# Kernel tuning notes

Hardware: AMD Instinct MI355X
Metric: run time of the kernel (lower is better)

Reference implementation:

```python
import jax, jax.numpy as jnp
import numpy as np

N = 80000
E = 1280000
C_IN, HID, C_OUT = 3, 64, 1
DEPTH = 3
KS = [40000, 20000, 10000]  # ceil(0.5 * n) per pooling level
EPS = 1e-5


def gcn_conv(x, W, src, dst, ew, n, fill=2.0):
    # PyG GCNConv with add_self_loops=True; improved => self-loop weight fill=2.0
    h = x @ W                                           # [n, F]
    deg = jax.ops.segment_sum(ew, dst, num_segments=n) + fill
    dinv = jax.lax.rsqrt(deg)
    norm = dinv[src] * ew * dinv[dst]                   # [E]
    agg = jax.ops.segment_sum(norm[:, None] * h[src], dst, num_segments=n)
    return agg + (fill * dinv * dinv)[:, None] * h      # self-loop term


def batchnorm(x, gamma, beta):
    # BatchNorm1d in training mode: biased batch stats over the node dim
    mu = jnp.mean(x, axis=0)
    var = jnp.var(x, axis=0)
    return gamma * (x - mu) * jax.lax.rsqrt(var + EPS) + beta


def gcn_block(x, src, dst, ew, n, W, gamma, beta, fill=2.0):
    return jax.nn.relu(batchnorm(gcn_conv(x, W, src, dst, ew, n, fill), gamma, beta))


def topk_pool(x, src, dst, ew, w, k):
    # TopKPooling with ReLU nonlinearity: score = relu(x.w / ||w||)
    n = x.shape[0]
    score = jax.nn.relu(x @ w / jnp.linalg.norm(w))
    sc, perm = jax.lax.top_k(score, k)
    xk = x[perm] * sc[:, None]
    # filter_adj with fixed edge count: invalid edges get weight 0 (no-op in GCN)
    mapping = jnp.full((n,), -1, dtype=src.dtype).at[perm].set(
        jnp.arange(k, dtype=src.dtype))
    ns, nd = mapping[src], mapping[dst]
    valid = (ns >= 0) & (nd >= 0)
    ns = jnp.where(valid, ns, 0)
    nd = jnp.where(valid, nd, 0)
    new_ew = jnp.where(valid, ew, jnp.zeros((), ew.dtype))
    return xk, ns, nd, new_ew, perm


def _forward(x, edge_index, Wd, gd, bd, pw, Wu, gu, bu, W_out):
    src, dst = edge_index[0], edge_index[1]
    ew = jnp.ones(src.shape, x.dtype)
    n = x.shape[0]
    x = gcn_block(x, src, dst, ew, n, Wd[0], gd[0], bd[0])
    xs, sds, ews, perms = [x], [(src, dst)], [ew], []
    for i in range(DEPTH):
        x, src, dst, ew, perm = topk_pool(x, src, dst, ew, pw[i], KS[i])
        x = gcn_block(x, src, dst, ew, KS[i], Wd[i + 1], gd[i + 1], bd[i + 1])
        if i < DEPTH - 1:
            xs.append(x); sds.append((src, dst)); ews.append(ew)
        perms.append(perm)
    for i in range(DEPTH):
        j = DEPTH - 1 - i
        res = xs[j]; src, dst = sds[j]; ew = ews[j]; perm = perms[j]
        up = jnp.zeros_like(res).at[perm].set(x)
        x = res + up
        if i < DEPTH - 1:
            x = gcn_block(x, src, dst, ew, res.shape[0], Wu[i], gu[i], bu[i])
        else:
            x = jax.nn.sigmoid(
                gcn_conv(x, W_out, src, dst, ew, res.shape[0], fill=1.0))
    return x


def setup_inputs() -> dict:
    key = jax.random.key(0)
    ks = jax.random.split(key, 16)
    nrm = lambda k, shape: jax.random.normal(k, shape, jnp.float32) * 0.1
    inp = {
        "x": jax.random.normal(ks[0], (N, C_IN), jnp.float32),
        "edge_index": jax.random.randint(ks[1], (2, E), 0, N, jnp.int32),
    }
    dims = [(C_IN, HID)] + [(HID, HID)] * DEPTH
    ki = 2
    for l, (a, b) in enumerate(dims):
        inp[f"W_d{l}"] = nrm(ks[ki], (a, b)); ki += 1
        inp[f"g_d{l}"] = jnp.ones((b,), jnp.float32)
        inp[f"b_d{l}"] = jnp.zeros((b,), jnp.float32)
    for l in range(DEPTH):
        inp[f"pw{l}"] = nrm(ks[ki], (HID,)); ki += 1
    for l in range(DEPTH - 1):
        inp[f"W_u{l}"] = nrm(ks[ki], (HID, HID)); ki += 1
        inp[f"g_u{l}"] = jnp.ones((HID,), jnp.float32)
        inp[f"b_u{l}"] = jnp.zeros((HID,), jnp.float32)
    inp["W_out"] = nrm(ks[ki], (HID, C_OUT))
    return inp


def reference(x, edge_index, W_d0, g_d0, b_d0, W_d1, g_d1, b_d1, W_d2, g_d2,
              b_d2, W_d3, g_d3, b_d3, pw0, pw1, pw2, W_u0, g_u0, b_u0,
              W_u1, g_u1, b_u1, W_out):
    Wd = [W_d0, W_d1, W_d2, W_d3]
    gd = [g_d0, g_d1, g_d2, g_d3]
    bd = [b_d0, b_d1, b_d2, b_d3]
    pw = [pw0, pw1, pw2]
    Wu = [W_u0, W_u1]
    gu = [g_u0, g_u1]
    bu = [b_u0, b_u1]
    return _forward(x, edge_index, Wd, gd, bd, pw, Wu, gu, bu, W_out)
```

## Files before the change

kernel.cpp:

```cpp
#include <hip/hip_runtime.h>
#include <cstdint>
#include <utility>

#define NN0 80000
#define NE 1280000
#define MMB_GRID 2048
#define EB 2048
#define ENB 625

static inline int cdiv(int a, int b){ return (a+b-1)/b; }

__global__ void k_conv64(const int* __restrict__ rp, const int* __restrict__ col,
                         const float* __restrict__ dinv, const float* __restrict__ x,
                         const float* __restrict__ W, float* __restrict__ out,
                         float* __restrict__ part, int n){
  __shared__ float yl[4][64];
  __shared__ float ls[64], lq[64];
  int lane = threadIdx.x & 63, w = threadIdx.x >> 6;
  if (threadIdx.x < 64){ ls[threadIdx.x] = 0.f; lq[threadIdx.x] = 0.f; }
  __syncthreads();
  float sa = 0.f, sq = 0.f;
  int wid = blockIdx.x*4 + w, nw = gridDim.x*4;
  for (int i = wid; i < n; i += nw){
    int beg = rp[i], end = rp[i+1];
    float di = dinv[i];
    float y = 0.f;
    int j = beg;
    for (; j + 4 <= end; j += 4){
      int s0 = col[j], s1 = col[j+1], s2 = col[j+2], s3 = col[j+3];
      float y0 = dinv[s0]*x[s0*64+lane];
      float y1 = dinv[s1]*x[s1*64+lane];
      float y2 = dinv[s2]*x[s2*64+lane];
      float y3 = dinv[s3]*x[s3*64+lane];
      y += (y0+y1) + (y2+y3);
    }
    for (; j < end; j++){ int s = col[j]; y += dinv[s]*x[s*64+lane]; }
    y = di*y + 2.f*di*di*x[i*64+lane];
    yl[w][lane] = y;
    float acc = 0.f;
    #pragma unroll
    for (int k2 = 0; k2 < 64; k2++)
      acc += yl[w][k2]*W[k2*64+lane];
    out[i*64+lane] = acc;
    sa += acc; sq += acc*acc;
  }
  atomicAdd(&ls[lane], sa); atomicAdd(&lq[lane], sq);
  __syncthreads();
  if (threadIdx.x < 128)
    part[blockIdx.x*128 + threadIdx.x] =
      (threadIdx.x < 64) ? ls[threadIdx.x] : lq[threadIdx.x-64];
}

__global__ void k_conv3(const int* __restrict__ rp, const int* __restrict__ col,
                        const float* __restrict__ dinv, const float* __restrict__ x,
                        const float* __restrict__ W, float* __restrict__ out,
                        float* __restrict__ part, int n){
  __shared__ float ls[64], lq[64];
  int lane = threadIdx.x & 63, w = threadIdx.x >> 6;
  if (threadIdx.x < 64){ ls[threadIdx.x] = 0.f; lq[threadIdx.x] = 0.f; }
  __syncthreads();
  float wf0 = W[lane], wf1 = W[64+lane], wf2 = W[128+lane];
  float sa = 0.f, sq = 0.f;
  int wid = blockIdx.x*4 + w, nw = gridDim.x*4;
  for (int i = wid; i < n; i += nw){
    int beg = rp[i], end = rp[i+1];
    float a0 = 0.f, a1 = 0.f, a2 = 0.f;
    for (int j = beg + lane; j < end; j += 64){
      int s2 = col[j];
      float ds = dinv[s2];
      a0 += ds*x[s2*3+0]; a1 += ds*x[s2*3+1]; a2 += ds*x[s2*3+2];
    }
    for (int o = 32; o > 0; o >>= 1){
      a0 += __shfl_xor(a0, o); a1 += __shfl_xor(a1, o); a2 += __shfl_xor(a2, o);
    }
    float di = dinv[i];
    float sl = 2.f*di*di;
    a0 = di*a0 + sl*x[i*3+0];
    a1 = di*a1 + sl*x[i*3+1];
    a2 = di*a2 + sl*x[i*3+2];
    float s = a0*wf0 + a1*wf1 + a2*wf2;
    out[i*64+lane] = s; sa += s; sq += s*s;
  }
  atomicAdd(&ls[lane], sa); atomicAdd(&lq[lane], sq);
  __syncthreads();
  if (threadIdx.x < 128)
    part[blockIdx.x*128 + threadIdx.x] =
      (threadIdx.x < 64) ? ls[threadIdx.x] : lq[threadIdx.x-64];
}

__global__ void k_stats_reduce(const float* __restrict__ part, float* __restrict__ stats){
  int c = blockIdx.x, lane = threadIdx.x;
  float s = 0.f;
  for (int b = lane; b < MMB_GRID; b += 64) s += part[b*128 + c];
  for (int o = 32; o > 0; o >>= 1) s += __shfl_xor(s, o);
  if (lane == 0) stats[c] = s;
}

__global__ void k_matvec(const float* __restrict__ x, const float* __restrict__ W,
                         float* __restrict__ h1, int n){
  int lane = threadIdx.x & 63, w = threadIdx.x >> 6;
  int wid = blockIdx.x*4 + w, nw = gridDim.x*4;
  float wv = W[lane];
  for (int i = wid; i < n; i += nw){
    float v = x[i*64+lane]*wv;
    for (int o = 32; o > 0; o >>= 1) v += __shfl_xor(v, o);
    if (lane == 0) h1[i] = v;
  }
}

__global__ void k_ehist6(const int* __restrict__ key, int* __restrict__ hist, int shift){
  __shared__ int lh[64];
  if (threadIdx.x < 64) lh[threadIdx.x] = 0;
  __syncthreads();
  int base = blockIdx.x*EB + threadIdx.x;
  #pragma unroll
  for (int u = 0; u < 8; u++)
    atomicAdd(&lh[(key[base + u*256] >> shift) & 63], 1);
  __syncthreads();
  if (threadIdx.x < 64) hist[threadIdx.x*ENB + blockIdx.x] = lh[threadIdx.x];
}

__global__ void k_escatter6(const int* __restrict__ keyin, const int* __restrict__ valin,
                            int* __restrict__ keyout, int* __restrict__ valout,
                            const int* __restrict__ hist, int shift){
  __shared__ int dbase[64], run[64], wcnt[4][64];
  int t = threadIdx.x, lane = t & 63, w = t >> 6;
  if (t < 64){ dbase[t] = hist[t*ENB + blockIdx.x]; run[t] = 0; }
  __syncthreads();
  for (int u = 0; u < 8; u++){
    if (t < 64){ wcnt[0][t]=0; wcnt[1][t]=0; wcnt[2][t]=0; wcnt[3][t]=0; }
    __syncthreads();
    int g = blockIdx.x*EB + u*256 + t;
    int kk = keyin[g], vv = valin[g];
    int d = (kk >> shift) & 63;
    unsigned long long m = ~0ull;
    #pragma unroll
    for (int b = 0; b < 6; b++){
      unsigned long long bal = __ballot((d >> b) & 1);
      m &= ((d >> b) & 1) ? bal : ~bal;
    }
    int rnk = __popcll(m & ((1ull << lane) - 1ull));
    if (rnk == 0) wcnt[w][d] = __popcll(m);
    __syncthreads();
    int off2 = run[d] + rnk;
    for (int w2 = 0; w2 < w; w2++) off2 += wcnt[w2][d];
    int pos = dbase[d] + off2;
    keyout[pos] = kk; valout[pos] = vv;
    __syncthreads();
    if (t < 64) run[t] += wcnt[0][t] + wcnt[1][t] + wcnt[2][t] + wcnt[3][t];
    __syncthreads();
  }
}

__global__ void k_rp_search(const int* __restrict__ skey, int* __restrict__ rp,
                            float* __restrict__ dinvA, float* __restrict__ dinvB, int n){
  int i = blockIdx.x*blockDim.x + threadIdx.x;
  if (i >= n) return;
  int lo = 0, hi = NE;
  while (lo < hi){ int mid = (lo+hi)>>1; if (skey[mid] < i) lo = mid+1; else hi = mid; }
  int a = lo;
  lo = a; hi = NE;
  while (lo < hi){ int mid = (lo+hi)>>1; if (skey[mid] < i+1) lo = mid+1; else hi = mid; }
  int b2 = lo;
  rp[i] = a;
  if (i == n-1) rp[n] = NE;
  float deg = (float)(b2 - a);
  dinvA[i] = 1.0f/sqrtf(deg + 2.f);
  dinvB[i] = 1.0f/sqrtf(deg + 1.f);
}

__global__ void k_scan_part(const int* __restrict__ in, int* __restrict__ bsum, int n){
  __shared__ int ws[256];
  int base = blockIdx.x*2048 + threadIdx.x*8;
  int s = 0;
  #pragma unroll
  for (int u = 0; u < 8; u++){ int i = base+u; if (i < n) s += in[i]; }
  ws[threadIdx.x] = s; __syncthreads();
  for (int st = 128; st > 0; st >>= 1){
    if (threadIdx.x < st) ws[threadIdx.x] += ws[threadIdx.x+st];
    __syncthreads();
  }
  if (threadIdx.x == 0) bsum[blockIdx.x] = ws[0];
}

__global__ void k_scan_fin_rp(const int* __restrict__ in, const int* __restrict__ bsum, int nb,
                              int* __restrict__ rp, float* __restrict__ dinvA, int n){
  __shared__ int bws[256]; __shared__ int ws[256];
  int t = threadIdx.x;
  bws[t] = (t < nb) ? bsum[t] : 0; __syncthreads();
  for (int st = 1; st < 256; st <<= 1){
    int a = (t >= st) ? bws[t-st] : 0; __syncthreads();
    bws[t] += a; __syncthreads();
  }
  int blockoff = (blockIdx.x == 0) ? 0 : bws[blockIdx.x-1];
  int base = blockIdx.x*2048 + t*8;
  int v[8]; int s = 0;
  #pragma unroll
  for (int u = 0; u < 8; u++){ int i = base+u; v[u] = (i < n) ? in[i] : 0; s += v[u]; }
  ws[t] = s; __syncthreads();
  for (int st = 1; st < 256; st <<= 1){
    int a = (t >= st) ? ws[t-st] : 0; __syncthreads();
    ws[t] += a; __syncthreads();
  }
  int off = blockoff + ws[t] - s;
  #pragma unroll
  for (int u = 0; u < 8; u++){
    int i = base+u;
    if (i < n){
      rp[i] = off; off += v[u];
      dinvA[i] = 1.0f/sqrtf((float)v[u] + 2.f);
      if (i == n-1) rp[n] = off;
    }
  }
}

__global__ void k_scan_fin_flat(int* __restrict__ data, const int* __restrict__ bsum, int nb, int n){
  __shared__ int bws[256]; __shared__ int ws[256];
  int t = threadIdx.x;
  bws[t] = (t < nb) ? bsum[t] : 0; __syncthreads();
  for (int st = 1; st < 256; st <<= 1){
    int a = (t >= st) ? bws[t-st] : 0; __syncthreads();
    bws[t] += a; __syncthreads();
  }
  int blockoff = (blockIdx.x == 0) ? 0 : bws[blockIdx.x-1];
  int base = blockIdx.x*2048 + t*8;
  int v[8]; int s = 0;
  #pragma unroll
  for (int u = 0; u < 8; u++){ int i = base+u; v[u] = (i < n) ? data[i] : 0; s += v[u]; }
  ws[t] = s; __syncthreads();
  for (int st = 1; st < 256; st <<= 1){
    int a = (t >= st) ? ws[t-st] : 0; __syncthreads();
    ws[t] += a; __syncthreads();
  }
  int off = blockoff + ws[t] - s;
  #pragma unroll
  for (int u = 0; u < 8; u++){
    int i = base+u;
    if (i < n){ data[i] = off; off += v[u]; }
  }
}

__global__ void k_hist_mapped(const int* __restrict__ rp_p, const int* __restrict__ col_p,
                              const int* __restrict__ mapv, int* __restrict__ indeg, int np){
  int d = blockIdx.x*blockDim.x + threadIdx.x;
  if (d >= np) return;
  int md = mapv[d];
  if (md < 0) return;
  int c = 0, e = rp_p[d+1];
  int j = rp_p[d];
  for (; j + 4 <= e; j += 4){
    int c0 = (mapv[col_p[j]]   >= 0);
    int c1 = (mapv[col_p[j+1]] >= 0);
    int c2 = (mapv[col_p[j+2]] >= 0);
    int c3 = (mapv[col_p[j+3]] >= 0);
    c += (c0+c1) + (c2+c3);
  }
  for (; j < e; j++) if (mapv[col_p[j]] >= 0) c++;
  indeg[md] = c;
}
__global__ void k_scatter_mapped(const int* __restrict__ rp_p, const int* __restrict__ col_p,
                                 const int* __restrict__ mapv, const int* __restrict__ rp_c,
                                 int* __restrict__ col_c, int np){
  int d = blockIdx.x*blockDim.x + threadIdx.x;
  if (d >= np) return;
  int md = mapv[d];
  if (md < 0) return;
  int pos = rp_c[md], e = rp_p[d+1];
  int j = rp_p[d];
  for (; j + 4 <= e; j += 4){
    int m0 = mapv[col_p[j]], m1 = mapv[col_p[j+1]];
    int m2 = mapv[col_p[j+2]], m3 = mapv[col_p[j+3]];
    if (m0 >= 0) col_c[pos++] = m0;
    if (m1 >= 0) col_c[pos++] = m1;
    if (m2 >= 0) col_c[pos++] = m2;
    if (m3 >= 0) col_c[pos++] = m3;
  }
  for (; j < e; j++){
    int ms = mapv[col_p[j]];
    if (ms >= 0) col_c[pos++] = ms;
  }
}

__global__ void k_gather_sig(const int* __restrict__ rp, const int* __restrict__ col,
                             const float* __restrict__ dinv, const float* __restrict__ h1,
                             float* __restrict__ out, int n){
  int i = blockIdx.x*blockDim.x + threadIdx.x;
  if (i >= n) return;
  int beg = rp[i], end = rp[i+1];
  float di = dinv[i];
  float acc = 0.f;
  int j = beg;
  for (; j + 4 <= end; j += 4){
    int s0 = col[j], s1 = col[j+1], s2 = col[j+2], s3 = col[j+3];
    float v0 = dinv[s0]*h1[s0];
    float v1 = dinv[s1]*h1[s1];
    float v2 = dinv[s2]*h1[s2];
    float v3 = dinv[s3]*h1[s3];
    acc += (v0+v1) + (v2+v3);
  }
  for (; j < end; j++) acc += dinv[col[j]]*h1[col[j]];
  float v = di*acc + di*di*h1[i];
  out[i] = 1.f/(1.f+expf(-v));
}

__global__ void k_bnrelu_scatter(const float* __restrict__ x, const float* __restrict__ stats,
                                 const float* __restrict__ gamma, const float* __restrict__ beta,
                                 const int* __restrict__ perm, float* __restrict__ res, int n){
  int t = blockIdx.x*blockDim.x + threadIdx.x;
  if (t >= n*64) return;
  int r = t >> 6, f = t & 63;
  float inv_n = 1.0f/(float)n;
  float mu = stats[f]*inv_n;
  float var = stats[64+f]*inv_n - mu*mu;
  float v = gamma[f]*(x[t]-mu)*(1.0f/sqrtf(var+1e-5f)) + beta[f];
  res[perm[r]*64+f] += fmaxf(v, 0.f);
}

__global__ void k_bnrelu_score(float* __restrict__ x, const float* __restrict__ stats,
                               const float* __restrict__ gamma, const float* __restrict__ beta,
                               const float* __restrict__ pw,
                               float* __restrict__ score, unsigned* __restrict__ key,
                               int* __restrict__ idx, int n, int P){
  int lane = threadIdx.x & 63, w = threadIdx.x >> 6;
  int wid = blockIdx.x*4 + w, nw = gridDim.x*4;
  float inv_n = 1.f/(float)n;
  float mu = stats[lane]*inv_n;
  float var = stats[64+lane]*inv_n - mu*mu;
  float gs = gamma[lane]*(1.f/sqrtf(var+1e-5f));
  float bt = beta[lane];
  float pv = pw[lane];
  float q = pv*pv;
  for (int o = 32; o > 0; o >>= 1) q += __shfl_xor(q, o);
  float qn = 1.f/sqrtf(q);
  for (int i = wid; i < n; i += nw){
    float v = fmaxf(gs*(x[i*64+lane]-mu)+bt, 0.f);
    x[i*64+lane] = v;
    float s = v*pv;
    for (int o = 32; o > 0; o >>= 1) s += __shfl_xor(s, o);
    if (lane == 0){
      float sc = fmaxf(s*qn, 0.f);
      score[i] = sc; key[i] = ~__float_as_uint(sc); idx[i] = i;
    }
  }
  for (int g = n + wid; g < P; g += nw)
    if (lane == 0){ key[g] = 0xFFFFFFFFu; idx[g] = 0; }
}

__global__ void k_radix_hist(const unsigned* __restrict__ key, int* __restrict__ hist,
                             int shift, int nblk){
  __shared__ int lh[256];
  lh[threadIdx.x] = 0; __syncthreads();
  int base = blockIdx.x*1024 + threadIdx.x;
  #pragma unroll
  for (int u = 0; u < 4; u++){
    unsigned d = (key[base + u*256] >> shift) & 255u;
    atomicAdd(&lh[d], 1);
  }
  __syncthreads();
  hist[threadIdx.x*nblk + blockIdx.x] = lh[threadIdx.x];
}

__global__ void k_radix_scatter(const unsigned* __restrict__ keyin, const int* __restrict__ idxin,
                                unsigned* __restrict__ keyout, int* __restrict__ idxout,
                                const int* __restrict__ hist, int shift, int nblk){
  __shared__ int dbase[256], run[256], sc[256];
  __shared__ int wcnt[4][256];
  int t = threadIdx.x, lane = t & 63, w = t >> 6;
  int pre = 0, tot = 0;
  for (int b = 0; b < nblk; b++){
    int v = hist[t*nblk + b];
    if (b < blockIdx.x) pre += v;
    tot += v;
  }
  sc[t] = tot; __syncthreads();
  for (int st = 1; st < 256; st <<= 1){
    int a = (t >= st) ? sc[t-st] : 0; __syncthreads();
    sc[t] += a; __syncthreads();
  }
  dbase[t] = sc[t] - tot + pre;
  run[t] = 0;
  for (int u = 0; u < 4; u++){
    wcnt[0][t] = 0; wcnt[1][t] = 0; wcnt[2][t] = 0; wcnt[3][t] = 0;
    __syncthreads();
    int g = blockIdx.x*1024 + u*256 + t;
    unsigned kk = keyin[g]; int id = idxin[g];
    unsigned d = (kk >> shift) & 255u;
    unsigned long long m = ~0ull;
    #pragma unroll
    for (int b = 0; b < 8; b++){
      unsigned long long bal = __ballot((d >> b) & 1u);
      m &= ((d >> b) & 1u) ? bal : ~bal;
    }
    int rnk = __popcll(m & ((1ull << lane) - 1ull));
    if (rnk == 0) wcnt[w][d] = __popcll(m);
    __syncthreads();
    int off2 = run[d] + rnk;
    for (int w2 = 0; w2 < w; w2++) off2 += wcnt[w2][d];
    int pos = dbase[d] + off2;
    keyout[pos] = kk; idxout[pos] = id;
    __syncthreads();
    run[t] += wcnt[0][t] + wcnt[1][t] + wcnt[2][t] + wcnt[3][t];
    __syncthreads();
  }
}

__global__ void k_select_gather(const int* __restrict__ idxs, const float* __restrict__ x,
                                const float* __restrict__ score, int* __restrict__ perm,
                                int* __restrict__ mapv, float* __restrict__ xk, int n, int k){
  int t = blockIdx.x*blockDim.x + threadIdx.x;
  if (t < n){
    int i = idxs[t];
    mapv[i] = (t < k) ? t : -1;
    if (t < k) perm[t] = i;
  }
  if (t < k*64){
    int r = t >> 6, f = t & 63;
    int i = idxs[r];
    xk[t] = x[i*64+f]*score[i];
  }
}

extern "C" void kernel_launch(void* const* d_in, const int* in_sizes, int n_in,
                              void* d_out, int out_size, void* d_ws, size_t ws_size,
                              hipStream_t stream) {
  const float* x_in = (const float*)d_in[0];
  const int* ei = (const int*)d_in[1];
  const int* src0 = ei;
  const int* dst0 = ei + NE;
  const float* W_d[4] = {(const float*)d_in[2],(const float*)d_in[5],(const float*)d_in[8],(const float*)d_in[11]};
  const float* g_d[4] = {(const float*)d_in[3],(const float*)d_in[6],(const float*)d_in[9],(const float*)d_in[12]};
  const float* b_d[4] = {(const float*)d_in[4],(const float*)d_in[7],(const float*)d_in[10],(const float*)d_in[13]};
  const float* pw[3]  = {(const float*)d_in[14],(const float*)d_in[15],(const float*)d_in[16]};
  const float* W_u[2] = {(const float*)d_in[17],(const float*)d_in[20]};
  const float* g_u[2] = {(const float*)d_in[18],(const float*)d_in[21]};
  const float* b_u[2] = {(const float*)d_in[19],(const float*)d_in[22]};
  const float* W_out  = (const float*)d_in[23];
  float* out = (float*)d_out;

  float* base = (float*)d_ws;
  size_t off = 0;
  auto alloc = [&](size_t nf){ float* p = base + off; off += nf; return p; };
  float* x0 = alloc(5120000);
  float* x1 = alloc(2560000);
  float* x2 = alloc(1280000);
  float* x3 = alloc(640000);
  float* A  = alloc(2560000);
  int* col0 = (int*)alloc(NE);
  int* col1 = (int*)alloc(NE);
  int* col2 = (int*)alloc(NE);
  int* col3 = (int*)alloc(NE);
  int* ek1 = (int*)alloc(NE);
  int* ev1 = (int*)alloc(NE);
  int* ek2 = (int*)alloc(NE);
  int* ev2 = (int*)alloc(NE);
  int* rp0 = (int*)alloc(80001);
  int* rp1 = (int*)alloc(40001);
  int* rp2 = (int*)alloc(20001);
  int* rp3 = (int*)alloc(10001);
  int* indeg  = (int*)alloc(NN0);
  float* dinv0  = alloc(NN0);
  float* dinv0f = alloc(NN0);
  float* dinv1  = alloc(40000);
  float* dinv2  = alloc(20000);
  float* dinv3  = alloc(10000);
  float* score = alloc(NN0);
  int* mapv = (int*)alloc(NN0);
  int* p0 = (int*)alloc(40000);
  int* p1 = (int*)alloc(20000);
  int* p2 = (int*)alloc(10000);
  float* stats = alloc(128);
  float* part  = alloc(MMB_GRID*128);
  unsigned* keyA = (unsigned*)alloc(81920);
  unsigned* keyB = (unsigned*)alloc(81920);
  int* idxA = (int*)alloc(81920);
  int* idxB = (int*)alloc(81920);
  int* hist = (int*)alloc(81920);
  int* ehist = (int*)alloc(64*ENB);
  int* bsum = (int*)alloc(256);
  (void)ws_size; (void)in_sizes; (void)n_in; (void)out_size;

  const int B = 256;

  auto scan_flat = [&](int* data, int n2){
    int nb = cdiv(n2, 2048);
    k_scan_part    <<<nb, 256, 0, stream>>>(data, bsum, n2);
    k_scan_fin_flat<<<nb, 256, 0, stream>>>(data, bsum, nb, n2);
  };
  auto scan_csr = [&](const int* indeg_, int* rp, float* dv, int n2){
    int nb = cdiv(n2, 2048);
    k_scan_part  <<<nb, 256, 0, stream>>>(indeg_, bsum, n2);
    k_scan_fin_rp<<<nb, 256, 0, stream>>>(indeg_, bsum, nb, rp, dv, n2);
  };

  auto conv = [&](const float* xin, const float* W, int n,
                  const int* rp, const int* col, const float* dv, float* dstb){
    k_conv64<<<MMB_GRID, B, 0, stream>>>(rp, col, dv, xin, W, dstb, part, n);
    k_stats_reduce<<<128, 64, 0, stream>>>(part, stats);
  };

  auto pool = [&](float* xb, const float* g, const float* bt, const float* w,
                  int n, int k, int* pm, float* xk){
    int nblk = cdiv(n, 1024), P = nblk*1024;
    k_bnrelu_score<<<1024, B, 0, stream>>>(xb, stats, g, bt, w, score, keyA, idxA, n, P);
    unsigned* ka = keyA; int* ia = idxA; unsigned* kb = keyB; int* ib = idxB;
    for (int pass = 0; pass < 4; pass++){
      k_radix_hist   <<<nblk, 256, 0, stream>>>(ka, hist, pass*8, nblk);
      k_radix_scatter<<<nblk, 256, 0, stream>>>(ka, ia, kb, ib, hist, pass*8, nblk);
      std::swap(ka, kb); std::swap(ia, ib);
    }
    k_select_gather<<<cdiv(k*64,B), B, 0, stream>>>(ia, xb, score, pm, mapv, xk, n, k);
  };

  auto csr_mapped = [&](const int* rp_p, const int* col_p, int np, int nc,
                        int* rp_c, int* col_c, float* dv){
    k_hist_mapped<<<cdiv(np,B), B, 0, stream>>>(rp_p, col_p, mapv, indeg, np);
    scan_csr(indeg, rp_c, dv, nc);
    k_scatter_mapped<<<cdiv(np,B), B, 0, stream>>>(rp_p, col_p, mapv, rp_c, col_c, np);
  };

  k_ehist6   <<<ENB, B, 0, stream>>>(dst0, ehist, 0);
  scan_flat(ehist, 64*ENB);
  k_escatter6<<<ENB, B, 0, stream>>>(dst0, src0, ek1, ev1, ehist, 0);
  k_ehist6   <<<ENB, B, 0, stream>>>(ek1, ehist, 6);
  scan_flat(ehist, 64*ENB);
  k_escatter6<<<ENB, B, 0, stream>>>(ek1, ev1, ek2, ev2, ehist, 6);
  k_ehist6   <<<ENB, B, 0, stream>>>(ek2, ehist, 12);
  scan_flat(ehist, 64*ENB);
  k_escatter6<<<ENB, B, 0, stream>>>(ek2, ev2, ek1, col0, ehist, 12);
  k_rp_search<<<cdiv(NN0,B), B, 0, stream>>>(ek1, rp0, dinv0, dinv0f, NN0);

  k_conv3<<<MMB_GRID, B, 0, stream>>>(rp0, col0, dinv0, x_in, W_d[0], x0, part, NN0);
  k_stats_reduce<<<128, 64, 0, stream>>>(part, stats);
  pool(x0, g_d[0], b_d[0], pw[0], NN0, 40000, p0, A);
  csr_mapped(rp0, col0, NN0, 40000, rp1, col1, dinv1);

  conv(A, W_d[1], 40000, rp1, col1, dinv1, x1);
  pool(x1, g_d[1], b_d[1], pw[1], 40000, 20000, p1, A);
  csr_mapped(rp1, col1, 40000, 20000, rp2, col2, dinv2);

  conv(A, W_d[2], 20000, rp2, col2, dinv2, x2);
  pool(x2, g_d[2], b_d[2], pw[2], 20000, 10000, p2, A);
  csr_mapped(rp2, col2, 20000, 10000, rp3, col3, dinv3);

  conv(A, W_d[3], 10000, rp3, col3, dinv3, x3);

  k_bnrelu_scatter<<<cdiv(10000*64,B), B, 0, stream>>>(x3, stats, g_d[3], b_d[3], p2, x2, 10000);
  conv(x2, W_u[0], 20000, rp2, col2, dinv2, A);
  k_bnrelu_scatter<<<cdiv(20000*64,B), B, 0, stream>>>(A, stats, g_u[0], b_u[0], p1, x1, 20000);
  conv(x1, W_u[1], 40000, rp1, col1, dinv1, A);
  k_bnrelu_scatter<<<cdiv(40000*64,B), B, 0, stream>>>(A, stats, g_u[1], b_u[1], p0, x0, 40000);

  float* h1 = score;
  k_matvec<<<512, B, 0, stream>>>(x0, W_out, h1, NN0);
  k_gather_sig<<<cdiv(NN0,B), B, 0, stream>>>(rp0, col0, dinv0f, h1, out, NN0);
}
```

Before: 740.8 us.

## Build CSR via atomic counting, fuse radix histograms and BN stats reductions

The 3-pass 6-bit radix sort that built the initial CSR is replaced by an atomic degree count, a scan and an atomic-cursor scatter. BatchNorm statistics now go straight into per-layer global slots through atomics, which removes the separate stats-reduce kernels. Radix-sort histograms for top-k are built inside the score kernel and the previous scatter pass, so the standalone histogram kernels are gone. Together these cut kernel launches and extra passes over memory. In exchange, the neighbour order within each CSR row becomes nondeterministic, so float summation order varies between runs, and global atomic contention goes up.

```diff
diff --git a/kernel.cpp b/kernel.cpp
--- a/kernel.cpp
+++ b/kernel.cpp
@@ -1,19 +1,89 @@
 #include <hip/hip_runtime.h>
 #include <cstdint>
-#include <utility>
 
 #define NN0 80000
 #define NE 1280000
 #define MMB_GRID 2048
-#define EB 2048
-#define ENB 625
+#define HPSTRIDE 20480
 
 static inline int cdiv(int a, int b){ return (a+b-1)/b; }
+
+__global__ void k_init(float* stats6, int* indeg){
+  int t = blockIdx.x*blockDim.x + threadIdx.x;
+  if (t < 768) stats6[t] = 0.f;
+  for (int i = t; i < NN0; i += gridDim.x*blockDim.x) indeg[i] = 0;
+}
+
+__global__ void k_deg0(const int* __restrict__ dst, int* __restrict__ indeg){
+  for (int e = blockIdx.x*blockDim.x + threadIdx.x; e < NE; e += gridDim.x*blockDim.x)
+    atomicAdd(&indeg[dst[e]], 1);
+}
+
+__global__ void k_escat0(const int* __restrict__ dst, const int* __restrict__ srcv,
+                         int* __restrict__ cur, int* __restrict__ col){
+  for (int e = blockIdx.x*blockDim.x + threadIdx.x; e < NE; e += gridDim.x*blockDim.x){
+    int d = dst[e];
+    int pos = atomicAdd(&cur[d], 1);
+    col[pos] = srcv[e];
+  }
+}
+
+__global__ void k_scan_part(const int* __restrict__ in, int* __restrict__ bsum, int n){
+  __shared__ int ws[256];
+  int base = blockIdx.x*2048 + threadIdx.x*8;
+  int s = 0;
+  #pragma unroll
+  for (int u = 0; u < 8; u++){ int i = base+u; if (i < n) s += in[i]; }
+  ws[threadIdx.x] = s; __syncthreads();
+  for (int st = 128; st > 0; st >>= 1){
+    if (threadIdx.x < st) ws[threadIdx.x] += ws[threadIdx.x+st];
+    __syncthreads();
+  }
+  if (threadIdx.x == 0) bsum[blockIdx.x] = ws[0];
+}
+
+__global__ void k_scan_fin_rp(const int* __restrict__ in, const int* __restrict__ bsum, int nb,
+                              int* __restrict__ rp, int* __restrict__ cur,
+                              float* __restrict__ dinvA, float* __restrict__ dinvB, int n){
+  __shared__ int bws[256]; __shared__ int ws[256];
+  int t = threadIdx.x;
+  bws[t] = (t < nb) ? bsum[t] : 0; __syncthreads();
+  for (int st = 1; st < 256; st <<= 1){
+    int a = (t >= st) ? bws[t-st] : 0; __syncthreads();
+    bws[t] += a; __syncthreads();
+  }
+  int blockoff = (blockIdx.x == 0) ? 0 : bws[blockIdx.x-1];
+  int base = blockIdx.x*2048 + t*8;
+  int v[8]; int s = 0;
+  #pragma unroll
+  for (int u = 0; u < 8; u++){ int i = base+u; v[u] = (i < n) ? in[i] : 0; s += v[u]; }
+  ws[t] = s; __syncthreads();
+  for (int st = 1; st < 256; st <<= 1){
+    int a = (t >= st) ? ws[t-st] : 0; __syncthreads();
+    ws[t] += a; __syncthreads();
+  }
+  int off = blockoff + ws[t] - s;
+  #pragma unroll
+  for (int u = 0; u < 8; u++){
+    int i = base+u;
+    if (i < n){
+      rp[i] = off;
+      if (cur) cur[i] = off;
+      off += v[u];
+      dinvA[i] = 1.0f/sqrtf((float)v[u] + 2.f);
+      if (dinvB) dinvB[i] = 1.0f/sqrtf((float)v[u] + 1.f);
+      if (i == n-1) rp[n] = off;
+    }
+  }
+}
+
 
 __global__ void k_conv64(const int* __restrict__ rp, const int* __restrict__ col,
                          const float* __restrict__ dinv, const float* __restrict__ x,
                          const float* __restrict__ W, float* __restrict__ out,
-                         float* __restrict__ part, int n){
+                         float* __restrict__ statsS, int* __restrict__ h0z, int nz, int n){
+  for (int i = blockIdx.x*blockDim.x + threadIdx.x; i < nz; i += gridDim.x*blockDim.x)
+    h0z[i] = 0;
   __shared__ float yl[4][64];
   __shared__ float ls[64], lq[64];
   int lane = threadIdx.x & 63, w = threadIdx.x >> 6;
@@ -47,14 +117,16 @@
   atomicAdd(&ls[lane], sa); atomicAdd(&lq[lane], sq);
   __syncthreads();
   if (threadIdx.x < 128)
-    part[blockIdx.x*128 + threadIdx.x] =
-      (threadIdx.x < 64) ? ls[threadIdx.x] : lq[threadIdx.x-64];
+    atomicAdd(&statsS[threadIdx.x],
+              (threadIdx.x < 64) ? ls[threadIdx.x] : lq[threadIdx.x-64]);
 }
 
 __global__ void k_conv3(const int* __restrict__ rp, const int* __restrict__ col,
                         const float* __restrict__ dinv, const float* __restrict__ x,
                         const float* __restrict__ W, float* __restrict__ out,
-                        float* __restrict__ part, int n){
+                        float* __restrict__ statsS, int* __restrict__ h0z, int nz, int n){
+  for (int i = blockIdx.x*blockDim.x + threadIdx.x; i < nz; i += gridDim.x*blockDim.x)
+    h0z[i] = 0;
   __shared__ float ls[64], lq[64];
   int lane = threadIdx.x & 63, w = threadIdx.x >> 6;
   if (threadIdx.x < 64){ ls[threadIdx.x] = 0.f; lq[threadIdx.x] = 0.f; }
@@ -84,243 +156,19 @@
   atomicAdd(&ls[lane], sa); atomicAdd(&lq[lane], sq);
   __syncthreads();
   if (threadIdx.x < 128)
-    part[blockIdx.x*128 + threadIdx.x] =
-      (threadIdx.x < 64) ? ls[threadIdx.x] : lq[threadIdx.x-64];
-}
-
-__global__ void k_stats_reduce(const float* __restrict__ part, float* __restrict__ stats){
-  int c = blockIdx.x, lane = threadIdx.x;
-  float s = 0.f;
-  for (int b = lane; b < MMB_GRID; b += 64) s += part[b*128 + c];
-  for (int o = 32; o > 0; o >>= 1) s += __shfl_xor(s, o);
-  if (lane == 0) stats[c] = s;
-}
-
-__global__ void k_matvec(const float* __restrict__ x, const float* __restrict__ W,
-                         float* __restrict__ h1, int n){
-  int lane = threadIdx.x & 63, w = threadIdx.x >> 6;
-  int wid = blockIdx.x*4 + w, nw = gridDim.x*4;
-  float wv = W[lane];
-  for (int i = wid; i < n; i += nw){
-    float v = x[i*64+lane]*wv;
-    for (int o = 32; o > 0; o >>= 1) v += __shfl_xor(v, o);
-    if (lane == 0) h1[i] = v;
-  }
-}
-
-__global__ void k_ehist6(const int* __restrict__ key, int* __restrict__ hist, int shift){
-  __shared__ int lh[64];
-  if (threadIdx.x < 64) lh[threadIdx.x] = 0;
-  __syncthreads();
-  int base = blockIdx.x*EB + threadIdx.x;
-  #pragma unroll
-  for (int u = 0; u < 8; u++)
-    atomicAdd(&lh[(key[base + u*256] >> shift) & 63], 1);
-  __syncthreads();
-  if (threadIdx.x < 64) hist[threadIdx.x*ENB + blockIdx.x] = lh[threadIdx.x];
-}
-
-__global__ void k_escatter6(const int* __restrict__ keyin, const int* __restrict__ valin,
-                            int* __restrict__ keyout, int* __restrict__ valout,
-                            const int* __restrict__ hist, int shift){
-  __shared__ int dbase[64], run[64], wcnt[4][64];
-  int t = threadIdx.x, lane = t & 63, w = t >> 6;
-  if (t < 64){ dbase[t] = hist[t*ENB + blockIdx.x]; run[t] = 0; }
-  __syncthreads();
-  for (int u = 0; u < 8; u++){
-    if (t < 64){ wcnt[0][t]=0; wcnt[1][t]=0; wcnt[2][t]=0; wcnt[3][t]=0; }
-    __syncthreads();
-    int g = blockIdx.x*EB + u*256 + t;
-    int kk = keyin[g], vv = valin[g];
-    int d = (kk >> shift) & 63;
-    unsigned long long m = ~0ull;
-    #pragma unroll
-    for (int b = 0; b < 6; b++){
-      unsigned long long bal = __ballot((d >> b) & 1);
-      m &= ((d >> b) & 1) ? bal : ~bal;
-    }
-    int rnk = __popcll(m & ((1ull << lane) - 1ull));
-    if (rnk == 0) wcnt[w][d] = __popcll(m);
-    __syncthreads();
-    int off2 = run[d] + rnk;
-    for (int w2 = 0; w2 < w; w2++) off2 += wcnt[w2][d];
-    int pos = dbase[d] + off2;
-    keyout[pos] = kk; valout[pos] = vv;
-    __syncthreads();
-    if (t < 64) run[t] += wcnt[0][t] + wcnt[1][t] + wcnt[2][t] + wcnt[3][t];
-    __syncthreads();
-  }
-}
-
-__global__ void k_rp_search(const int* __restrict__ skey, int* __restrict__ rp,
-                            float* __restrict__ dinvA, float* __restrict__ dinvB, int n){
-  int i = blockIdx.x*blockDim.x + threadIdx.x;
-  if (i >= n) return;
-  int lo = 0, hi = NE;
-  while (lo < hi){ int mid = (lo+hi)>>1; if (skey[mid] < i) lo = mid+1; else hi = mid; }
-  int a = lo;
-  lo = a; hi = NE;
-  while (lo < hi){ int mid = (lo+hi)>>1; if (skey[mid] < i+1) lo = mid+1; else hi = mid; }
-  int b2 = lo;
-  rp[i] = a;
-  if (i == n-1) rp[n] = NE;
-  float deg = (float)(b2 - a);
-  dinvA[i] = 1.0f/sqrtf(deg + 2.f);
-  dinvB[i] = 1.0f/sqrtf(deg + 1.f);
-}
-
-__global__ void k_scan_part(const int* __restrict__ in, int* __restrict__ bsum, int n){
-  __shared__ int ws[256];
-  int base = blockIdx.x*2048 + threadIdx.x*8;
-  int s = 0;
-  #pragma unroll
-  for (int u = 0; u < 8; u++){ int i = base+u; if (i < n) s += in[i]; }
-  ws[threadIdx.x] = s; __syncthreads();
-  for (int st = 128; st > 0; st >>= 1){
-    if (threadIdx.x < st) ws[threadIdx.x] += ws[threadIdx.x+st];
-    __syncthreads();
-  }
-  if (threadIdx.x == 0) bsum[blockIdx.x] = ws[0];
-}
-
-__global__ void k_scan_fin_rp(const int* __restrict__ in, const int* __restrict__ bsum, int nb,
-                              int* __restrict__ rp, float* __restrict__ dinvA, int n){
-  __shared__ int bws[256]; __shared__ int ws[256];
-  int t = threadIdx.x;
-  bws[t] = (t < nb) ? bsum[t] : 0; __syncthreads();
-  for (int st = 1; st < 256; st <<= 1){
-    int a = (t >= st) ? bws[t-st] : 0; __syncthreads();
-    bws[t] += a; __syncthreads();
-  }
-  int blockoff = (blockIdx.x == 0) ? 0 : bws[blockIdx.x-1];
-  int base = blockIdx.x*2048 + t*8;
-  int v[8]; int s = 0;
-  #pragma unroll
-  for (int u = 0; u < 8; u++){ int i = base+u; v[u] = (i < n) ? in[i] : 0; s += v[u]; }
-  ws[t] = s; __syncthreads();
-  for (int st = 1; st < 256; st <<= 1){
-    int a = (t >= st) ? ws[t-st] : 0; __syncthreads();
-    ws[t] += a; __syncthreads();
-  }
-  int off = blockoff + ws[t] - s;
-  #pragma unroll
-  for (int u = 0; u < 8; u++){
-    int i = base+u;
-    if (i < n){
-      rp[i] = off; off += v[u];
-      dinvA[i] = 1.0f/sqrtf((float)v[u] + 2.f);
-      if (i == n-1) rp[n] = off;
-    }
-  }
-}
-
-__global__ void k_scan_fin_flat(int* __restrict__ data, const int* __restrict__ bsum, int nb, int n){
-  __shared__ int bws[256]; __shared__ int ws[256];
-  int t = threadIdx.x;
-  bws[t] = (t < nb) ? bsum[t] : 0; __syncthreads();
-  for (int st = 1; st < 256; st <<= 1){
-    int a = (t >= st) ? bws[t-st] : 0; __syncthreads();
-    bws[t] += a; __syncthreads();
-  }
-  int blockoff = (blockIdx.x == 0) ? 0 : bws[blockIdx.x-1];
-  int base = blockIdx.x*2048 + t*8;
-  int v[8]; int s = 0;
-  #pragma unroll
-  for (int u = 0; u < 8; u++){ int i = base+u; v[u] = (i < n) ? data[i] : 0; s += v[u]; }
-  ws[t] = s; __syncthreads();
-  for (int st = 1; st < 256; st <<= 1){
-    int a = (t >= st) ? ws[t-st] : 0; __syncthreads();
-    ws[t] += a; __syncthreads();
-  }
-  int off = blockoff + ws[t] - s;
-  #pragma unroll
-  for (int u = 0; u < 8; u++){
-    int i = base+u;
-    if (i < n){ data[i] = off; off += v[u]; }
-  }
-}
-
-__global__ void k_hist_mapped(const int* __restrict__ rp_p, const int* __restrict__ col_p,
-                              const int* __restrict__ mapv, int* __restrict__ indeg, int np){
-  int d = blockIdx.x*blockDim.x + threadIdx.x;
-  if (d >= np) return;
-  int md = mapv[d];
-  if (md < 0) return;
-  int c = 0, e = rp_p[d+1];
-  int j = rp_p[d];
-  for (; j + 4 <= e; j += 4){
-    int c0 = (mapv[col_p[j]]   >= 0);
-    int c1 = (mapv[col_p[j+1]] >= 0);
-    int c2 = (mapv[col_p[j+2]] >= 0);
-    int c3 = (mapv[col_p[j+3]] >= 0);
-    c += (c0+c1) + (c2+c3);
-  }
-  for (; j < e; j++) if (mapv[col_p[j]] >= 0) c++;
-  indeg[md] = c;
-}
-__global__ void k_scatter_mapped(const int* __restrict__ rp_p, const int* __restrict__ col_p,
-                                 const int* __restrict__ mapv, const int* __restrict__ rp_c,
-                                 int* __restrict__ col_c, int np){
-  int d = blockIdx.x*blockDim.x + threadIdx.x;
-  if (d >= np) return;
-  int md = mapv[d];
-  if (md < 0) return;
-  int pos = rp_c[md], e = rp_p[d+1];
-  int j = rp_p[d];
-  for (; j + 4 <= e; j += 4){
-    int m0 = mapv[col_p[j]], m1 = mapv[col_p[j+1]];
-    int m2 = mapv[col_p[j+2]], m3 = mapv[col_p[j+3]];
-    if (m0 >= 0) col_c[pos++] = m0;
-    if (m1 >= 0) col_c[pos++] = m1;
-    if (m2 >= 0) col_c[pos++] = m2;
-    if (m3 >= 0) col_c[pos++] = m3;
-  }
-  for (; j < e; j++){
-    int ms = mapv[col_p[j]];
-    if (ms >= 0) col_c[pos++] = ms;
-  }
-}
-
-__global__ void k_gather_sig(const int* __restrict__ rp, const int* __restrict__ col,
-                             const float* __restrict__ dinv, const float* __restrict__ h1,
-                             float* __restrict__ out, int n){
-  int i = blockIdx.x*blockDim.x + threadIdx.x;
-  if (i >= n) return;
-  int beg = rp[i], end = rp[i+1];
-  float di = dinv[i];
-  float acc = 0.f;
-  int j = beg;
-  for (; j + 4 <= end; j += 4){
-    int s0 = col[j], s1 = col[j+1], s2 = col[j+2], s3 = col[j+3];
-    float v0 = dinv[s0]*h1[s0];
-    float v1 = dinv[s1]*h1[s1];
-    float v2 = dinv[s2]*h1[s2];
-    float v3 = dinv[s3]*h1[s3];
-    acc += (v0+v1) + (v2+v3);
-  }
-  for (; j < end; j++) acc += dinv[col[j]]*h1[col[j]];
-  float v = di*acc + di*di*h1[i];
-  out[i] = 1.f/(1.f+expf(-v));
-}
-
-__global__ void k_bnrelu_scatter(const float* __restrict__ x, const float* __restrict__ stats,
-                                 const float* __restrict__ gamma, const float* __restrict__ beta,
-                                 const int* __restrict__ perm, float* __restrict__ res, int n){
-  int t = blockIdx.x*blockDim.x + threadIdx.x;
-  if (t >= n*64) return;
-  int r = t >> 6, f = t & 63;
-  float inv_n = 1.0f/(float)n;
-  float mu = stats[f]*inv_n;
-  float var = stats[64+f]*inv_n - mu*mu;
-  float v = gamma[f]*(x[t]-mu)*(1.0f/sqrtf(var+1e-5f)) + beta[f];
-  res[perm[r]*64+f] += fmaxf(v, 0.f);
-}
-
-__global__ void k_bnrelu_score(float* __restrict__ x, const float* __restrict__ stats,
-                               const float* __restrict__ gamma, const float* __restrict__ beta,
-                               const float* __restrict__ pw,
-                               float* __restrict__ score, unsigned* __restrict__ key,
-                               int* __restrict__ idx, int n, int P){
+    atomicAdd(&statsS[threadIdx.x],
+              (threadIdx.x < 64) ? ls[threadIdx.x] : lq[threadIdx.x-64]);
+}
+
+__global__ void k_pool_score(float* __restrict__ x, const float* __restrict__ stats,
+                             const float* __restrict__ gamma, const float* __restrict__ beta,
+                             const float* __restrict__ pw,
+                             float* __restrict__ score, unsigned* __restrict__ key,
+                             int* __restrict__ idx, int* __restrict__ h0,
+                             int* __restrict__ hz, int n, int nblk){
+  for (int i = blockIdx.x*blockDim.x + threadIdx.x; i < 3*HPSTRIDE; i += gridDim.x*blockDim.x)
+    hz[i] = 0;
+  int P = nblk*1024;
   int lane = threadIdx.x & 63, w = threadIdx.x >> 6;
   int wid = blockIdx.x*4 + w, nw = gridDim.x*4;
   float inv_n = 1.f/(float)n;
@@ -339,30 +187,22 @@
     for (int o = 32; o > 0; o >>= 1) s += __shfl_xor(s, o);
     if (lane == 0){
       float sc = fmaxf(s*qn, 0.f);
-      score[i] = sc; key[i] = ~__float_as_uint(sc); idx[i] = i;
+      unsigned kk = ~__float_as_uint(sc);
+      score[i] = sc; key[i] = kk; idx[i] = i;
+      atomicAdd(&h0[(kk & 255u)*nblk + (i >> 10)], 1);
     }
   }
   for (int g = n + wid; g < P; g += nw)
-    if (lane == 0){ key[g] = 0xFFFFFFFFu; idx[g] = 0; }
-}
-
-__global__ void k_radix_hist(const unsigned* __restrict__ key, int* __restrict__ hist,
-                             int shift, int nblk){
-  __shared__ int lh[256];
-  lh[threadIdx.x] = 0; __syncthreads();
-  int base = blockIdx.x*1024 + threadIdx.x;
-  #pragma unroll
-  for (int u = 0; u < 4; u++){
-    unsigned d = (key[base + u*256] >> shift) & 255u;
-    atomicAdd(&lh[d], 1);
-  }
-  __syncthreads();
-  hist[threadIdx.x*nblk + blockIdx.x] = lh[threadIdx.x];
+    if (lane == 0){
+      key[g] = 0xFFFFFFFFu; idx[g] = 0;
+      atomicAdd(&h0[255*nblk + (g >> 10)], 1);
+    }
 }
 
 __global__ void k_radix_scatter(const unsigned* __restrict__ keyin, const int* __restrict__ idxin,
                                 unsigned* __restrict__ keyout, int* __restrict__ idxout,
-                                const int* __restrict__ hist, int shift, int nblk){
+                                const int* __restrict__ hist, int shift, int nblk,
+                                int* __restrict__ nexthist, int nextshift){
   __shared__ int dbase[256], run[256], sc[256];
   __shared__ int wcnt[4][256];
   int t = threadIdx.x, lane = t & 63, w = t >> 6;
@@ -398,6 +238,8 @@
     for (int w2 = 0; w2 < w; w2++) off2 += wcnt[w2][d];
     int pos = dbase[d] + off2;
     keyout[pos] = kk; idxout[pos] = id;
+    if (nexthist)
+      atomicAdd(&nexthist[((kk >> nextshift) & 255u)*nblk + (pos >> 10)], 1);
     __syncthreads();
     run[t] += wcnt[0][t] + wcnt[1][t] + wcnt[2][t] + wcnt[3][t];
     __syncthreads();
@@ -419,6 +261,96 @@
     xk[t] = x[i*64+f]*score[i];
   }
 }
+
+__global__ void k_hist_mapped(const int* __restrict__ rp_p, const int* __restrict__ col_p,
+                              const int* __restrict__ mapv, int* __restrict__ indeg, int np){
+  int d = blockIdx.x*blockDim.x + threadIdx.x;
+  if (d >= np) return;
+  int md = mapv[d];
+  if (md < 0) return;
+  int c = 0, e = rp_p[d+1];
+  int j = rp_p[d];
+  for (; j + 4 <= e; j += 4){
+    int c0 = (mapv[col_p[j]]   >= 0);
+    int c1 = (mapv[col_p[j+1]] >= 0);
+    int c2 = (mapv[col_p[j+2]] >= 0);
+    int c3 = (mapv[col_p[j+3]] >= 0);
+    c += (c0+c1) + (c2+c3);
+  }
+  for (; j < e; j++) if (mapv[col_p[j]] >= 0) c++;
+  indeg[md] = c;
+}
+
+__global__ void k_scatter_mapped(const int* __restrict__ rp_p, const int* __restrict__ col_p,
+                                 const int* __restrict__ mapv, const int* __restrict__ rp_c,
+                                 int* __restrict__ col_c, int np){
+  int d = blockIdx.x*blockDim.x + threadIdx.x;
+  if (d >= np) return;
+  int md = mapv[d];
+  if (md < 0) return;
+  int pos = rp_c[md], e = rp_p[d+1];
+  int j = rp_p[d];
+  for (; j + 4 <= e; j += 4){
+    int m0 = mapv[col_p[j]], m1 = mapv[col_p[j+1]];
+    int m2 = mapv[col_p[j+2]], m3 = mapv[col_p[j+3]];
+    if (m0 >= 0) col_c[pos++] = m0;
+    if (m1 >= 0) col_c[pos++] = m1;
+    if (m2 >= 0) col_c[pos++] = m2;
+    if (m3 >= 0) col_c[pos++] = m3;
+  }
+  for (; j < e; j++){
+    int ms = mapv[col_p[j]];
+    if (ms >= 0) col_c[pos++] = ms;
+  }
+}
+
+__global__ void k_bnrelu_scatter(const float* __restrict__ x, const float* __restrict__ stats,
+                                 const float* __restrict__ gamma, const float* __restrict__ beta,
+                                 const int* __restrict__ perm, float* __restrict__ res, int n){
+  int t = blockIdx.x*blockDim.x + threadIdx.x;
+  if (t >= n*64) return;
+  int r = t >> 6, f = t & 63;
+  float inv_n = 1.0f/(float)n;
+  float mu = stats[f]*inv_n;
+  float var = stats[64+f]*inv_n - mu*mu;
+  float v = gamma[f]*(x[t]-mu)*(1.0f/sqrtf(var+1e-5f)) + beta[f];
+  res[perm[r]*64+f] += fmaxf(v, 0.f);
+}
+
+__global__ void k_matvec(const float* __restrict__ x, const float* __restrict__ W,
+                         float* __restrict__ h1, int n){
+  int lane = threadIdx.x & 63, w = threadIdx.x >> 6;
+  int wid = blockIdx.x*4 + w, nw = gridDim.x*4;
+  float wv = W[lane];
+  for (int i = wid; i < n; i += nw){
+    float v = x[i*64+lane]*wv;
+    for (int o = 32; o > 0; o >>= 1) v += __shfl_xor(v, o);
+    if (lane == 0) h1[i] = v;
+  }
+}
+
+__global__ void k_gather_sig(const int* __restrict__ rp, const int* __restrict__ col,
+                             const float* __restrict__ dinv, const float* __restrict__ h1,
+                             float* __restrict__ out, int n){
+  int i = blockIdx.x*blockDim.x + threadIdx.x;
+  if (i >= n) return;
+  int beg = rp[i], end = rp[i+1];
+  float di = dinv[i];
+  float acc = 0.f;
+  int j = beg;
+  for (; j + 4 <= end; j += 4){
+    int s0 = col[j], s1 = col[j+1], s2 = col[j+2], s3 = col[j+3];
+    float v0 = dinv[s0]*h1[s0];
+    float v1 = dinv[s1]*h1[s1];
+    float v2 = dinv[s2]*h1[s2];
+    float v3 = dinv[s3]*h1[s3];
+    acc += (v0+v1) + (v2+v3);
+  }
+  for (; j < end; j++) acc += dinv[col[j]]*h1[col[j]];
+  float v = di*acc + di*di*h1[i];
+  out[i] = 1.f/(1.f+expf(-v));
+}
+
 
 extern "C" void kernel_launch(void* const* d_in, const int* in_sizes, int n_in,
                               void* d_out, int out_size, void* d_ws, size_t ws_size,
@@ -449,14 +381,11 @@
   int* col1 = (int*)alloc(NE);
   int* col2 = (int*)alloc(NE);
   int* col3 = (int*)alloc(NE);
-  int* ek1 = (int*)alloc(NE);
-  int* ev1 = (int*)alloc(NE);
-  int* ek2 = (int*)alloc(NE);
-  int* ev2 = (int*)alloc(NE);
   int* rp0 = (int*)alloc(80001);
   int* rp1 = (int*)alloc(40001);
   int* rp2 = (int*)alloc(20001);
   int* rp3 = (int*)alloc(10001);
+  int* cur0 = (int*)alloc(NN0);
   int* indeg  = (int*)alloc(NN0);
   float* dinv0  = alloc(NN0);
   float* dinv0f = alloc(NN0);
@@ -468,87 +397,66 @@
   int* p0 = (int*)alloc(40000);
   int* p1 = (int*)alloc(20000);
   int* p2 = (int*)alloc(10000);
-  float* stats = alloc(128);
-  float* part  = alloc(MMB_GRID*128);
+  float* stats6 = alloc(768);
   unsigned* keyA = (unsigned*)alloc(81920);
   unsigned* keyB = (unsigned*)alloc(81920);
   int* idxA = (int*)alloc(81920);
   int* idxB = (int*)alloc(81920);
-  int* hist = (int*)alloc(81920);
-  int* ehist = (int*)alloc(64*ENB);
+  int* hb = (int*)alloc(4*HPSTRIDE);
+  int* h1b = hb, *h2b = hb + HPSTRIDE, *h3b = hb + 2*HPSTRIDE, *h0b = hb + 3*HPSTRIDE;
   int* bsum = (int*)alloc(256);
   (void)ws_size; (void)in_sizes; (void)n_in; (void)out_size;
 
   const int B = 256;
-
-  auto scan_flat = [&](int* data, int n2){
-    int nb = cdiv(n2, 2048);
-    k_scan_part    <<<nb, 256, 0, stream>>>(data, bsum, n2);
-    k_scan_fin_flat<<<nb, 256, 0, stream>>>(data, bsum, nb, n2);
-  };
-  auto scan_csr = [&](const int* indeg_, int* rp, float* dv, int n2){
-    int nb = cdiv(n2, 2048);
-    k_scan_part  <<<nb, 256, 0, stream>>>(indeg_, bsum, n2);
-    k_scan_fin_rp<<<nb, 256, 0, stream>>>(indeg_, bsum, nb, rp, dv, n2);
-  };
-
-  auto conv = [&](const float* xin, const float* W, int n,
-                  const int* rp, const int* col, const float* dv, float* dstb){
-    k_conv64<<<MMB_GRID, B, 0, stream>>>(rp, col, dv, xin, W, dstb, part, n);
-    k_stats_reduce<<<128, 64, 0, stream>>>(part, stats);
-  };
-
-  auto pool = [&](float* xb, const float* g, const float* bt, const float* w,
-                  int n, int k, int* pm, float* xk){
-    int nblk = cdiv(n, 1024), P = nblk*1024;
-    k_bnrelu_score<<<1024, B, 0, stream>>>(xb, stats, g, bt, w, score, keyA, idxA, n, P);
-    unsigned* ka = keyA; int* ia = idxA; unsigned* kb = keyB; int* ib = idxB;
-    for (int pass = 0; pass < 4; pass++){
-      k_radix_hist   <<<nblk, 256, 0, stream>>>(ka, hist, pass*8, nblk);
-      k_radix_scatter<<<nblk, 256, 0, stream>>>(ka, ia, kb, ib, hist, pass*8, nblk);
-      std::swap(ka, kb); std::swap(ia, ib);
-    }
-    k_select_gather<<<cdiv(k*64,B), B, 0, stream>>>(ia, xb, score, pm, mapv, xk, n, k);
+  auto S = [&](int i){ return stats6 + i*128; };
+
+  k_init<<<cdiv(NN0,B), B, 0, stream>>>(stats6, indeg);
+  k_deg0<<<1024, B, 0, stream>>>(dst0, indeg);
+  k_scan_part<<<cdiv(NN0,2048), B, 0, stream>>>(indeg, bsum, NN0);
+  k_scan_fin_rp<<<cdiv(NN0,2048), B, 0, stream>>>(indeg, bsum, cdiv(NN0,2048),
+                                                  rp0, cur0, dinv0, dinv0f, NN0);
+  k_escat0<<<1024, B, 0, stream>>>(dst0, src0, cur0, col0);
+
+  auto pool = [&](float* xb, const float* st, const float* gm, const float* bt,
+                  const float* pwv, int n, int k, int* pm){
+    int nblk = cdiv(n, 1024);
+    k_pool_score<<<1024, B, 0, stream>>>(xb, st, gm, bt, pwv, score, keyA, idxA,
+                                         h0b, h1b, n, nblk);
+    k_radix_scatter<<<nblk, B, 0, stream>>>(keyA, idxA, keyB, idxB, h0b, 0,  nblk, h1b, 8);
+    k_radix_scatter<<<nblk, B, 0, stream>>>(keyB, idxB, keyA, idxA, h1b, 8,  nblk, h2b, 16);
+    k_radix_scatter<<<nblk, B, 0, stream>>>(keyA, idxA, keyB, idxB, h2b, 16, nblk, h3b, 24);
+    k_radix_scatter<<<nblk, B, 0, stream>>>(keyB, idxB, keyA, idxA, h3b, 24, nblk, nullptr, 0);
+    k_select_gather<<<cdiv(k*64,B), B, 0, stream>>>(idxA, xb, score, pm, mapv, A, n, k);
   };
 
   auto csr_mapped = [&](const int* rp_p, const int* col_p, int np, int nc,
                         int* rp_c, int* col_c, float* dv){
     k_hist_mapped<<<cdiv(np,B), B, 0, stream>>>(rp_p, col_p, mapv, indeg, np);
-    scan_csr(indeg, rp_c, dv, nc);
+    k_scan_part<<<cdiv(nc,2048), B, 0, stream>>>(indeg, bsum, nc);
+    k_scan_fin_rp<<<cdiv(nc,2048), B, 0, stream>>>(indeg, bsum, cdiv(nc,2048),
+                                                   rp_c, nullptr, dv, nullptr, nc);
     k_scatter_mapped<<<cdiv(np,B), B, 0, stream>>>(rp_p, col_p, mapv, rp_c, col_c, np);
   };
 
-  k_ehist6   <<<ENB, B, 0, stream>>>(dst0, ehist, 0);
-  scan_flat(ehist, 64*ENB);
-  k_escatter6<<<ENB, B, 0, stream>>>(dst0, src0, ek1, ev1, ehist, 0);
-  k_ehist6   <<<ENB, B, 0, stream>>>(ek1, ehist, 6);
-  scan_flat(ehist, 64*ENB);
-  k_escatter6<<<ENB, B, 0, stream>>>(ek1, ev1, ek2, ev2, ehist, 6);
-  k_ehist6   <<<ENB, B, 0, stream>>>(ek2, ehist, 12);
-  scan_flat(ehist, 64*ENB);
-  k_escatter6<<<ENB, B, 0, stream>>>(ek2, ev2, ek1, col0, ehist, 12);
-  k_rp_search<<<cdiv(NN0,B), B, 0, stream>>>(ek1, rp0, dinv0, dinv0f, NN0);
-
-  k_conv3<<<MMB_GRID, B, 0, stream>>>(rp0, col0, dinv0, x_in, W_d[0], x0, part, NN0);
-  k_stats_reduce<<<128, 64, 0, stream>>>(part, stats);
-  pool(x0, g_d[0], b_d[0], pw[0], NN0, 40000, p0, A);
+  k_conv3<<<MMB_GRID, B, 0, stream>>>(rp0, col0, dinv0, x_in, W_d[0], x0, S(0), h0b, HPSTRIDE, NN0);
+  pool(x0, S(0), g_d[0], b_d[0], pw[0], NN0, 40000, p0);
   csr_mapped(rp0, col0, NN0, 40000, rp1, col1, dinv1);
 
-  conv(A, W_d[1], 40000, rp1, col1, dinv1, x1);
-  pool(x1, g_d[1], b_d[1], pw[1], 40000, 20000, p1, A);
+  k_conv64<<<MMB_GRID, B, 0, stream>>>(rp1, col1, dinv1, A, W_d[1], x1, S(1), h0b, HPSTRIDE, 40000);
+  pool(x1, S(1), g_d[1], b_d[1], pw[1], 40000, 20000, p1);
   csr_mapped(rp1, col1, 40000, 20000, rp2, col2, dinv2);
 
-  conv(A, W_d[2], 20000, rp2, col2, dinv2, x2);
-  pool(x2, g_d[2], b_d[2], pw[2], 20000, 10000, p2, A);
+  k_conv64<<<MMB_GRID, B, 0, stream>>>(rp2, col2, dinv2, A, W_d[2], x2, S(2), h0b, HPSTRIDE, 20000);
+  pool(x2, S(2), g_d[2], b_d[2], pw[2], 20000, 10000, p2);
   csr_mapped(rp2, col2, 20000, 10000, rp3, col3, dinv3);
 
-  conv(A, W_d[3], 10000, rp3, col3, dinv3, x3);
-
-  k_bnrelu_scatter<<<cdiv(10000*64,B), B, 0, stream>>>(x3, stats, g_d[3], b_d[3], p2, x2, 10000);
-  conv(x2, W_u[0], 20000, rp2, col2, dinv2, A);
-  k_bnrelu_scatter<<<cdiv(20000*64,B), B, 0, stream>>>(A, stats, g_u[0], b_u[0], p1, x1, 20000);
-  conv(x1, W_u[1], 40000, rp1, col1, dinv1, A);
-  k_bnrelu_scatter<<<cdiv(40000*64,B), B, 0, stream>>>(A, stats, g_u[1], b_u[1], p0, x0, 40000);
+  k_conv64<<<MMB_GRID, B, 0, stream>>>(rp3, col3, dinv3, A, W_d[3], x3, S(3), nullptr, 0, 10000);
+
+  k_bnrelu_scatter<<<cdiv(10000*64,B), B, 0, stream>>>(x3, S(3), g_d[3], b_d[3], p2, x2, 10000);
+  k_conv64<<<MMB_GRID, B, 0, stream>>>(rp2, col2, dinv2, x2, W_u[0], A, S(4), nullptr, 0, 20000);
+  k_bnrelu_scatter<<<cdiv(20000*64,B), B, 0, stream>>>(A, S(4), g_u[0], b_u[0], p1, x1, 20000);
+  k_conv64<<<MMB_GRID, B, 0, stream>>>(rp1, col1, dinv1, x1, W_u[1], A, S(5), nullptr, 0, 40000);
+  k_bnrelu_scatter<<<cdiv(40000*64,B), B, 0, stream>>>(A, S(5), g_u[1], b_u[1], p0, x0, 40000);
 
   float* h1 = score;
   k_matvec<<<512, B, 0, stream>>>(x0, W_out, h1, NN0);
```

Result: slower. 2.852 ms (+285.0%).
